# Kernel tuning notes

Hardware: AMD Instinct MI355X
Metric: run time of the kernel (lower is better)

## Reference

```python
import jax, jax.numpy as jnp
import numpy as np

B, T, M, D, H, DK, DV = 2, 1024, 1024, 1024, 16, 64, 64
R = 2 * T + M  # number of relative positions required by rel_shift path


def setup_inputs() -> dict:
    key = jax.random.key(0)
    ks = jax.random.split(key, 11)
    s = 0.02
    return {
        "inputs": jax.random.normal(ks[0], (B, T, D), jnp.float32),
        "attention_mask": jnp.ones((B, T, M + T), jnp.float32),
        "positional_encodings": jax.random.normal(ks[1], (R, D), jnp.float32),
        "memory": jax.random.normal(ks[2], (B, M, D), jnp.float32),
        "Wq": jax.random.normal(ks[3], (D, H * DK), jnp.float32) * s,
        "Wk": jax.random.normal(ks[4], (D, H * DK), jnp.float32) * s,
        "Wv": jax.random.normal(ks[5], (D, H * DV), jnp.float32) * s,
        "Wr": jax.random.normal(ks[6], (D, H * DK), jnp.float32) * s,
        "r_w_bias": jax.random.normal(ks[7], (H, DK), jnp.float32) * s,
        "r_r_bias": jax.random.normal(ks[8], (H, DK), jnp.float32) * s,
        "W_out": jax.random.normal(ks[9], (H * DV, D), jnp.float32) * s,
    }


def _rel_shift(m, attention_length):
    # m: [T_q, T_q + L] -> [T_q, L], TXL relative shift via reshape/slice
    tq, total = m.shape
    x = m.reshape(total, tq)[1:].reshape(tq, total - 1)
    return x[:, :attention_length]


def reference(inputs, attention_mask, positional_encodings, memory,
              Wq, Wk, Wv, Wr, r_w_bias, r_r_bias, W_out):
    b, t, d = inputs.shape
    values = jnp.concatenate([memory, inputs], axis=1)  # [B, L, D]
    L = values.shape[1]
    q = (inputs @ Wq).reshape(b, t, H, DK)
    k = (values @ Wk).reshape(b, L, H, DK)
    v = (values @ Wv).reshape(b, L, H, DV)
    rk = (positional_encodings @ Wr).reshape(-1, H, DK)  # [R, H, DK]
    # content + relative logits (TXL)
    content = jnp.einsum('bthd,bThd->bhtT', q + r_w_bias, k)        # [B,H,T,L]
    rel = jnp.einsum('bthd,rhd->bhtr', q + r_r_bias, rk)            # [B,H,T,R]
    rel = jax.vmap(jax.vmap(lambda m: _rel_shift(m, L)))(rel)       # [B,H,T,L]
    logits = (content + rel) * (DK ** -0.5)
    masked = logits - (1.0 - attention_mask[:, None, :, :]) * 1e30
    w = jax.nn.softmax(masked, axis=-1)
    attn = jnp.einsum('bhtT,bThd->bthd', w, v)                      # [B,T,H,DV]
    return attn.reshape(b, t, H * DV) @ W_out
```

## Files before the change

### kernel.cpp

```cpp
#include <hip/hip_runtime.h>
#include <stdint.h>

#define Bz 2
#define Tq 1024
#define Mm 1024
#define Hh 16
#define Ll 2048
#define Rr 3072

typedef __attribute__((ext_vector_type(8))) short bf16x8;
typedef __attribute__((ext_vector_type(4))) float f32x4;

typedef __attribute__((address_space(3))) uint8_t lds_u8_t;
typedef __attribute__((address_space(1))) uint8_t glb_u8_t;

__device__ __forceinline__ void gl2lds16(const void* g, void* l) {
  __builtin_amdgcn_global_load_lds((const glb_u8_t*)g, (lds_u8_t*)l, 16, 0, 0);
}

__device__ __forceinline__ unsigned short f2bf(float f) {
  unsigned int u = __builtin_bit_cast(unsigned int, f);
  u = u + 0x7fffu + ((u >> 16) & 1u);
  return (unsigned short)(u >> 16);
}
__device__ __forceinline__ float b2f(unsigned short s) {
  unsigned int u = ((unsigned int)s) << 16;
  return __builtin_bit_cast(float, u);
}

__global__ __launch_bounds__(256) void k_prep(const float* __restrict__ x,
                                              const float* __restrict__ mem,
                                              const float* __restrict__ pos,
                                              const float* __restrict__ mask,
                                              unsigned short* __restrict__ vin,
                                              unsigned short* __restrict__ pb,
                                              unsigned short* __restrict__ mb) {
  int bid = blockIdx.x;
  if (bid < 4096) {
    int idx = bid * 256 + threadIdx.x;
    int e = idx << 2;
    int row = e >> 10, col = e & 1023;
    int b = row >> 11, l = row & 2047;
    const float* s = (l < Mm) ? (mem + (((size_t)b * Mm + l) << 10) + col)
                              : (x + (((size_t)b * Tq + (l - Mm)) << 10) + col);
    float4 v = *(const float4*)s;
    ushort4 o;
    o.x = f2bf(v.x); o.y = f2bf(v.y); o.z = f2bf(v.z); o.w = f2bf(v.w);
    *(ushort4*)(vin + e) = o;
  } else if (bid < 7168) {
    int idx = (bid - 4096) * 256 + threadIdx.x;
    int e = idx << 2;
    float4 v = *(const float4*)(pos + e);
    ushort4 t;
    t.x = f2bf(v.x); t.y = f2bf(v.y); t.z = f2bf(v.z); t.w = f2bf(v.w);
    *(ushort4*)(pb + e) = t;
  } else {
    int idx = (bid - 7168) * 256 + threadIdx.x;
    int e = idx << 2;
    const float BIGM = 1.442695e30f;
    float4 v = *(const float4*)(mask + e);
    ushort4 t;
    t.x = f2bf((1.0f - v.x) * BIGM); t.y = f2bf((1.0f - v.y) * BIGM);
    t.z = f2bf((1.0f - v.z) * BIGM); t.w = f2bf((1.0f - v.w) * BIGM);
    *(ushort4*)(mb + e) = t;
  }
}

__global__ __launch_bounds__(256) void k_wtall(
    const float* __restrict__ w0, const float* __restrict__ w1,
    const float* __restrict__ w2, const float* __restrict__ w3,
    const float* __restrict__ w4,
    unsigned short* __restrict__ t0, unsigned short* __restrict__ t1,
    unsigned short* __restrict__ t2, unsigned short* __restrict__ t3,
    unsigned short* __restrict__ t4) {
  const float* W;
  unsigned short* WT;
  switch (blockIdx.z) {
    case 0: W = w0; WT = t0; break;
    case 1: W = w1; WT = t1; break;
    case 2: W = w2; WT = t2; break;
    case 3: W = w3; WT = t3; break;
    default: W = w4; WT = t4; break;
  }
  __shared__ float tile[64][65];
  int k0 = blockIdx.x * 64, n0 = blockIdx.y * 64;
  int tid = threadIdx.x;
  int rr = tid >> 4, c4 = (tid & 15) * 4;
#pragma unroll
  for (int it = 0; it < 4; ++it) {
    int r = rr + it * 16;
    float4 v = *(const float4*)(W + (size_t)(k0 + r) * 1024 + n0 + c4);
    tile[r][c4] = v.x; tile[r][c4 + 1] = v.y;
    tile[r][c4 + 2] = v.z; tile[r][c4 + 3] = v.w;
  }
  __syncthreads();
#pragma unroll
  for (int it = 0; it < 4; ++it) {
    int n = rr + it * 16;
    ushort4 o;
    o.x = f2bf(tile[c4 + 0][n]); o.y = f2bf(tile[c4 + 1][n]);
    o.z = f2bf(tile[c4 + 2][n]); o.w = f2bf(tile[c4 + 3][n]);
    *(ushort4*)(WT + (size_t)(n0 + n) * 1024 + k0 + c4) = o;
  }
}

template <int RMAP>
__device__ __forceinline__ void gemm_core(const unsigned short* __restrict__ A,
                                          const unsigned short* __restrict__ Bt,
                                          int m0, int n0, unsigned short* As,
                                          unsigned short* Bs, f32x4 acc[4][4]) {
  const int tid = threadIdx.x;
  const int w = tid >> 6, lane = tid & 63;
  const int quad = lane >> 4, li = lane & 15;
  const int wr = w >> 1, wc = w & 1;
  f32x4 z = {0.f, 0.f, 0.f, 0.f};
#pragma unroll
  for (int mi = 0; mi < 4; ++mi)
#pragma unroll
    for (int ni = 0; ni < 4; ++ni) acc[mi][ni] = z;

  const int rs = lane >> 2;
  const int cs = lane & 3;

  for (int k0 = 0; k0 < 1024; k0 += 32) {
    __syncthreads();
#pragma unroll
    for (int s = 0; s < 2; ++s) {
      int i = w * 2 + s;
      int r = i * 16 + rs;
      int c = cs ^ ((r >> 1) & 3);
      int ar = m0 + r;
      if (RMAP) ar = ar + 1024 + (ar & 1024);
      gl2lds16(A + (size_t)ar * 1024 + k0 + c * 8, (char*)As + i * 1024);
      int br = n0 + r;
      gl2lds16(Bt + (size_t)br * 1024 + k0 + c * 8, (char*)Bs + i * 1024);
    }
    __syncthreads();
    bf16x8 af[4], bfr[4];
#pragma unroll
    for (int mi = 0; mi < 4; ++mi) {
      int r = wr * 64 + mi * 16 + li;
      int ch = quad ^ ((r >> 1) & 3);
      af[mi] = *(const bf16x8*)((const char*)As + r * 64 + ch * 16);
    }
#pragma unroll
    for (int ni = 0; ni < 4; ++ni) {
      int r = wc * 64 + ni * 16 + li;
      int ch = quad ^ ((r >> 1) & 3);
      bfr[ni] = *(const bf16x8*)((const char*)Bs + r * 64 + ch * 16);
    }
#pragma unroll
    for (int mi = 0; mi < 4; ++mi)
#pragma unroll
      for (int ni = 0; ni < 4; ++ni)
        acc[mi][ni] = __builtin_amdgcn_mfma_f32_16x16x32_bf16(
            af[mi], bfr[ni], acc[mi][ni], 0, 0, 0);
  }
}

__global__ __launch_bounds__(256) void k_proj(
    const unsigned short* __restrict__ Vin, const unsigned short* __restrict__ Pb,
    const unsigned short* __restrict__ WqT, const unsigned short* __restrict__ WkT,
    const unsigned short* __restrict__ WvT, const unsigned short* __restrict__ WrT,
    const float* __restrict__ rwb, const float* __restrict__ rrb,
    unsigned short* __restrict__ qwb, unsigned short* __restrict__ qrb,
    unsigned short* __restrict__ kb, unsigned short* __restrict__ vtb,
    unsigned short* __restrict__ rkb) {
  __shared__ unsigned short As[128 * 32];
  __shared__ unsigned short Bs[128 * 32];
  const int t = blockIdx.x;
  const int tid = threadIdx.x, w = tid >> 6, lane = tid & 63;
  const int quad = lane >> 4, li = lane & 15, wr = w >> 1, wc = w & 1;
  f32x4 acc[4][4];

  if (t < 256) {
    int m0 = (t >> 3) * 128, n0 = (t & 7) * 128;
    gemm_core<0>(Vin, WkT, m0, n0, As, Bs, acc);
#pragma unroll
    for (int mi = 0; mi < 4; ++mi)
#pragma unroll
      for (int ni = 0; ni < 4; ++ni)
#pragma unroll
        for (int reg = 0; reg < 4; ++reg) {
          int rrow = m0 + wr * 64 + mi * 16 + quad * 4 + reg;
          int cc = n0 + wc * 64 + ni * 16 + li;
          kb[(size_t)rrow * 1024 + cc] = f2bf(acc[mi][ni][reg]);
        }
  } else if (t < 512) {
    int tt = t - 256;
    int m0 = (tt >> 3) * 128, n0 = (tt & 7) * 128;
    gemm_core<0>(Vin, WvT, m0, n0, As, Bs, acc);
#pragma unroll
    for (int mi = 0; mi < 4; ++mi)
#pragma unroll
      for (int ni = 0; ni < 4; ++ni) {
        int r0 = m0 + wr * 64 + mi * 16 + quad * 4;
        int b = r0 >> 11, l0 = r0 & 2047;
        int cc = n0 + wc * 64 + ni * 16 + li;
        ushort4 o;
        o.x = f2bf(acc[mi][ni][0]); o.y = f2bf(acc[mi][ni][1]);
        o.z = f2bf(acc[mi][ni][2]); o.w = f2bf(acc[mi][ni][3]);
        *(ushort4*)(vtb + ((size_t)(b * 1024 + cc)) * Ll + l0) = o;
      }
  } else if (t < 640) {
    int tt = t - 512;
    int m0 = (tt >> 3) * 128, n0 = (tt & 7) * 128;
    gemm_core<1>(Vin, WqT, m0, n0, As, Bs, acc);
#pragma unroll
    for (int mi = 0; mi < 4; ++mi)
#pragma unroll
      for (int ni = 0; ni < 4; ++ni) {
        int cc = n0 + wc * 64 + ni * 16 + li;
        float bw_ = rwb[cc], br_ = rrb[cc];
#pragma unroll
        for (int reg = 0; reg < 4; ++reg) {
          int rrow = m0 + wr * 64 + mi * 16 + quad * 4 + reg;
          size_t off = (size_t)rrow * 1024 + cc;
          qwb[off] = f2bf(acc[mi][ni][reg] + bw_);
          qrb[off] = f2bf(acc[mi][ni][reg] + br_);
        }
      }
  } else {
    int tt = t - 640;
    int m0 = (tt >> 3) * 128, n0 = (tt & 7) * 128;
    gemm_core<0>(Pb, WrT, m0, n0, As, Bs, acc);
#pragma unroll
    for (int mi = 0; mi < 4; ++mi)
#pragma unroll
      for (int ni = 0; ni < 4; ++ni)
#pragma unroll
        for (int reg = 0; reg < 4; ++reg) {
          int rrow = m0 + wr * 64 + mi * 16 + quad * 4 + reg;
          int cc = n0 + wc * 64 + ni * 16 + li;
          rkb[(size_t)rrow * 1024 + cc] = f2bf(acc[mi][ni][reg]);
        }
  }
}

__global__ __launch_bounds__(256) void k_gemm_out64(
    const unsigned short* __restrict__ attnb, const unsigned short* __restrict__ WoT,
    float* __restrict__ out) {
  __shared__ unsigned short As[64 * 32];
  __shared__ unsigned short Bs[128 * 32];
  int m0 = blockIdx.x * 64, n0 = blockIdx.y * 128;
  const int tid = threadIdx.x, w = tid >> 6, lane = tid & 63;
  const int quad = lane >> 4, li = lane & 15, wr = w >> 1, wc = w & 1;
  f32x4 z = {0.f, 0.f, 0.f, 0.f};
  f32x4 acc[2][4];
#pragma unroll
  for (int mi = 0; mi < 2; ++mi)
#pragma unroll
    for (int ni = 0; ni < 4; ++ni) acc[mi][ni] = z;
  const int rs = lane >> 2, cs = lane & 3;
  for (int k0 = 0; k0 < 1024; k0 += 32) {
    __syncthreads();
    {
      int r = w * 16 + rs;
      int c = cs ^ ((r >> 1) & 3);
      gl2lds16(attnb + (size_t)(m0 + r) * 1024 + k0 + c * 8, (char*)As + w * 1024);
    }
#pragma unroll
    for (int s = 0; s < 2; ++s) {
      int i = w * 2 + s;
      int r = i * 16 + rs;
      int c = cs ^ ((r >> 1) & 3);
      gl2lds16(WoT + (size_t)(n0 + r) * 1024 + k0 + c * 8, (char*)Bs + i * 1024);
    }
    __syncthreads();
    bf16x8 af[2], bfr[4];
#pragma unroll
    for (int mi = 0; mi < 2; ++mi) {
      int r = wr * 32 + mi * 16 + li;
      int ch = quad ^ ((r >> 1) & 3);
      af[mi] = *(const bf16x8*)((const char*)As + r * 64 + ch * 16);
    }
#pragma unroll
    for (int ni = 0; ni < 4; ++ni) {
      int r = wc * 64 + ni * 16 + li;
      int ch = quad ^ ((r >> 1) & 3);
      bfr[ni] = *(const bf16x8*)((const char*)Bs + r * 64 + ch * 16);
    }
#pragma unroll
    for (int mi = 0; mi < 2; ++mi)
#pragma unroll
      for (int ni = 0; ni < 4; ++ni)
        acc[mi][ni] = __builtin_amdgcn_mfma_f32_16x16x32_bf16(
            af[mi], bfr[ni], acc[mi][ni], 0, 0, 0);
  }
#pragma unroll
  for (int mi = 0; mi < 2; ++mi)
#pragma unroll
    for (int ni = 0; ni < 4; ++ni)
#pragma unroll
      for (int reg = 0; reg < 4; ++reg) {
        int rrow = m0 + wr * 32 + mi * 16 + quad * 4 + reg;
        int cc = n0 + wc * 64 + ni * 16 + li;
        out[(size_t)rrow * 1024 + cc] = acc[mi][ni][reg];
      }
}

__global__ __launch_bounds__(256, 3) void k_attn(
    const unsigned short* __restrict__ qw, const unsigned short* __restrict__ qr,
    const unsigned short* __restrict__ kb, const unsigned short* __restrict__ vt,
    const unsigned short* __restrict__ rkb, const unsigned short* __restrict__ mb,
    float* __restrict__ po, float* __restrict__ pl) {
  __shared__ unsigned short Ks[64 * 64];
  __shared__ unsigned short Vs[64 * 64];
  __shared__ unsigned short Rs[128 * 64];
  __shared__ unsigned short BndP[4][16 * 72];

  const int tid = threadIdx.x;
  const int w = tid >> 6, lane = tid & 63;
  const int quad = lane >> 4, li = lane & 15;
  const int qt = blockIdx.x, h = blockIdx.y;
  const int b = blockIdx.z >> 1, split = blockIdx.z & 1;
  const int t0blk = qt * 64;
  const int t0w = t0blk + w * 16;
  const int rboff = 48 - 16 * w;
  const int rbase0 = Tq - t0blk - 63 + (split << 10);

  bf16x8 aqw[2], aqr[2];
  {
    const unsigned short* p1 = qw + ((size_t)((b * Tq + t0w + li) * Hh + h)) * 64;
    aqw[0] = *(const bf16x8*)(p1 + quad * 8);
    aqw[1] = *(const bf16x8*)(p1 + 32 + quad * 8);
    const unsigned short* p2 = qr + ((size_t)((b * Tq + t0w + li) * Hh + h)) * 64;
    aqr[0] = *(const bf16x8*)(p2 + quad * 8);
    aqr[1] = *(const bf16x8*)(p2 + 32 + quad * 8);
  }

  f32x4 z = {0.f, 0.f, 0.f, 0.f};
  f32x4 o[4];
  o[0] = z; o[1] = z; o[2] = z; o[3] = z;
  f32x4 ol = z;

  const int srow = lane >> 3;
  const int scs = lane & 7;
  const float SC = 0.125f * 1.4426950408889634f;
  const short oneb = 0x3F80;
  const bf16x8 onesf = {oneb, oneb, oneb, oneb, oneb, oneb, oneb, oneb};

  unsigned short* pw = &BndP[w][0];

  for (int jt = 0; jt < 16; ++jt) {
    const int j0 = (split << 10) + jt * 64;
    __syncthreads();
#pragma unroll
    for (int s = 0; s < 2; ++s) {
      int i = w * 2 + s;
      int r = i * 8 + srow;
      int c = scs ^ (r & 7);
      gl2lds16(kb + ((size_t)((b * Ll + j0 + r) * Hh + h)) * 64 + c * 8,
               (char*)Ks + i * 1024);
      gl2lds16(vt + ((size_t)((b * Hh + h) * 64 + r)) * Ll + j0 + c * 8,
               (char*)Vs + i * 1024);
    }
    if (jt == 0) {
#pragma unroll
      for (int s = 0; s < 4; ++s) {
        int i = w * 4 + s;
        int r = i * 8 + srow;
        int gr = rbase0 + r;
        if (gr > Rr - 1) gr = Rr - 1;
        int c = scs ^ (r & 7);
        gl2lds16(rkb + ((size_t)gr * Hh + h) * 64 + c * 8, (char*)Rs + i * 1024);
      }
    } else {
      int ph0 = (64 * (jt + 1)) & 127;
#pragma unroll
      for (int s = 0; s < 2; ++s) {
        int i2 = w * 2 + s;
        int rr = i2 * 8 + srow;
        int gr = rbase0 + 64 * jt + 64 + rr;
        if (gr > Rr - 1) gr = Rr - 1;
        int c = scs ^ (rr & 7);
        gl2lds16(rkb + ((size_t)gr * Hh + h) * 64 + c * 8,
                 (char*)Rs + ph0 * 128 + i2 * 1024);
      }
    }
    __syncthreads();

    f32x4 sc[4];
    sc[0] = z; sc[1] = z; sc[2] = z; sc[3] = z;
#pragma unroll
    for (int ks = 0; ks < 2; ++ks)
#pragma unroll
      for (int nt = 0; nt < 4; ++nt) {
        int j = nt * 16 + li;
        int ch = (ks * 4 + quad) ^ (j & 7);
        bf16x8 kf = *(const bf16x8*)((const char*)Ks + j * 128 + ch * 16);
        sc[nt] = __builtin_amdgcn_mfma_f32_16x16x32_bf16(aqw[ks], kf, sc[nt], 0, 0, 0);
      }
    f32x4 bd[5];
    bd[0] = z; bd[1] = z; bd[2] = z; bd[3] = z; bd[4] = z;
#pragma unroll
    for (int ks = 0; ks < 2; ++ks)
#pragma unroll
      for (int nt = 0; nt < 5; ++nt) {
        int pr = (rboff + nt * 16 + li + 64 * jt) & 127;
        int ch = (ks * 4 + quad) ^ (pr & 7);
        bf16x8 rf = *(const bf16x8*)((const char*)Rs + pr * 128 + ch * 16);
        bd[nt] = __builtin_amdgcn_mfma_f32_16x16x32_bf16(aqr[ks], rf, bd[nt], 0, 0, 0);
      }
#pragma unroll
    for (int nt = 0; nt < 5; ++nt)
#pragma unroll
      for (int reg = 0; reg < 4; ++reg) {
        int row = quad * 4 + reg;
        int jj = nt * 16 + li + row - 15;
        if ((unsigned)jj < 64u) pw[row * 72 + jj] = f2bf(bd[nt][reg]);
      }
    __builtin_amdgcn_s_waitcnt(0xc07f);

    float pbuf[4][4];
    const unsigned short* mrow0 = mb + ((size_t)(b * Tq + t0w)) * Ll + j0;
#pragma unroll
    for (int nt = 0; nt < 4; ++nt)
#pragma unroll
      for (int reg = 0; reg < 4; ++reg) {
        int row = quad * 4 + reg;
        float rel = b2f(pw[row * 72 + nt * 16 + li]);
        float mv = b2f(mrow0[(size_t)row * Ll + nt * 16 + li]);
        float s = (sc[nt][reg] + rel) * SC - mv;
        pbuf[nt][reg] = exp2f(s);
      }
    asm volatile("" ::: "memory");
#pragma unroll
    for (int nt = 0; nt < 4; ++nt)
#pragma unroll
      for (int reg = 0; reg < 4; ++reg)
        pw[(quad * 4 + reg) * 72 + nt * 16 + li] = f2bf(pbuf[nt][reg]);
    __builtin_amdgcn_s_waitcnt(0xc07f);
#pragma unroll
    for (int ks = 0; ks < 2; ++ks) {
      bf16x8 ap = *(const bf16x8*)(pw + li * 72 + ks * 32 + quad * 8);
      ol = __builtin_amdgcn_mfma_f32_16x16x32_bf16(ap, onesf, ol, 0, 0, 0);
#pragma unroll
      for (int nt = 0; nt < 4; ++nt) {
        int dv = nt * 16 + li;
        int ch = (ks * 4 + quad) ^ (dv & 7);
        bf16x8 vf = *(const bf16x8*)((const char*)Vs + dv * 128 + ch * 16);
        o[nt] = __builtin_amdgcn_mfma_f32_16x16x32_bf16(ap, vf, o[nt], 0, 0, 0);
      }
    }
  }
  const int bs = (b * 2 + split) * 16 + h;
#pragma unroll
  for (int nt = 0; nt < 4; ++nt)
#pragma unroll
    for (int reg = 0; reg < 4; ++reg) {
      int trow = t0w + quad * 4 + reg;
      po[((size_t)bs * 1024 + trow) * 64 + nt * 16 + li] = o[nt][reg];
    }
  if (li == 0) {
#pragma unroll
    for (int reg = 0; reg < 4; ++reg) {
      int trow = t0w + quad * 4 + reg;
      pl[(size_t)bs * 1024 + trow] = ol[reg];
    }
  }
}

__global__ __launch_bounds__(256) void k_combine(
    const float* __restrict__ po, const float* __restrict__ pl,
    unsigned short* __restrict__ attnb) {
  int id = blockIdx.x * 256 + threadIdx.x;
  int dv4 = (id & 15) << 2;
  int t = (id >> 4) & 1023;
  int h = (id >> 14) & 15;
  int b = id >> 18;
  size_t r0 = ((size_t)((b * 2 + 0) * 16 + h)) * 1024 + t;
  size_t r1 = ((size_t)((b * 2 + 1) * 16 + h)) * 1024 + t;
  float inv = 1.0f / (pl[r0] + pl[r1]);
  float4 o0 = *(const float4*)(po + r0 * 64 + dv4);
  float4 o1 = *(const float4*)(po + r1 * 64 + dv4);
  ushort4 res;
  res.x = f2bf((o0.x + o1.x) * inv);
  res.y = f2bf((o0.y + o1.y) * inv);
  res.z = f2bf((o0.z + o1.z) * inv);
  res.w = f2bf((o0.w + o1.w) * inv);
  *(ushort4*)(attnb + ((size_t)(b * 1024 + t)) * 1024 + h * 64 + dv4) = res;
}

extern "C" void kernel_launch(void* const* d_in, const int* in_sizes, int n_in,
                              void* d_out, int out_size, void* d_ws, size_t ws_size,
                              hipStream_t stream) {
  const float* x = (const float*)d_in[0];
  const float* mask = (const float*)d_in[1];
  const float* pos = (const float*)d_in[2];
  const float* mem = (const float*)d_in[3];
  const float* Wq = (const float*)d_in[4];
  const float* Wk = (const float*)d_in[5];
  const float* Wv = (const float*)d_in[6];
  const float* Wr = (const float*)d_in[7];
  const float* rwb = (const float*)d_in[8];
  const float* rrb = (const float*)d_in[9];
  const float* Wo = (const float*)d_in[10];
  float* out = (float*)d_out;

  uint8_t* ws = (uint8_t*)d_ws;
  const size_t MB = 1024 * 1024;
  unsigned short* Vinb = (unsigned short*)(ws + 0);
  unsigned short* WqT = (unsigned short*)(ws + 8 * MB);
  unsigned short* WkT = (unsigned short*)(ws + 10 * MB);
  unsigned short* WvT = (unsigned short*)(ws + 12 * MB);
  unsigned short* WrT = (unsigned short*)(ws + 14 * MB);
  unsigned short* WoT = (unsigned short*)(ws + 16 * MB);
  unsigned short* Pb = (unsigned short*)(ws + 18 * MB);
  unsigned short* qwb = (unsigned short*)(ws + 24 * MB);
  unsigned short* qrb = (unsigned short*)(ws + 28 * MB);
  unsigned short* kb = (unsigned short*)(ws + 32 * MB);
  unsigned short* vtb = (unsigned short*)(ws + 40 * MB);
  unsigned short* rkb = (unsigned short*)(ws + 48 * MB);
  unsigned short* mbb = (unsigned short*)(ws + 54 * MB);
  float* po = (float*)(ws + 0);
  float* pl = (float*)(ws + 18 * MB);
  unsigned short* attnb = (unsigned short*)(ws + 19 * MB);

  hipLaunchKernelGGL(k_prep, dim3(11264), dim3(256), 0, stream,
                     x, mem, pos, mask, Vinb, Pb, mbb);
  hipLaunchKernelGGL(k_wtall, dim3(16, 16, 5), dim3(256), 0, stream,
                     Wq, Wk, Wv, Wr, Wo, WqT, WkT, WvT, WrT, WoT);
  hipLaunchKernelGGL(k_proj, dim3(832), dim3(256), 0, stream,
                     Vinb, Pb, WqT, WkT, WvT, WrT, rwb, rrb, qwb, qrb, kb, vtb, rkb);
  hipLaunchKernelGGL(k_attn, dim3(16, 16, 4), dim3(256), 0, stream,
                     qwb, qrb, kb, vtb, rkb, mbb, po, pl);
  hipLaunchKernelGGL(k_combine, dim3(2048), dim3(256), 0, stream, po, pl, attnb);
  hipLaunchKernelGGL(k_gemm_out64, dim3(32, 8), dim3(256), 0, stream,
                     attnb, WoT, out);
}
```

Baseline: 268.9 us.

## Fuse content and relative logits before LDS shift, compute softmax in A-operand layout

Content scores are rotated across lanes with shuffles so they line up with the shifted relative-position tile. The sum is then written to LDS once, as fp16, instead of writing only the relative part and reading it back. The exp2 and mask step now runs while the MFMA A-operand is loaded from LDS, using vectorised mask loads per row. This drops one LDS write/read round trip and a wait per tile, at the cost of extra shuffles and fp16 range limits on the pre-scaled logits.

```diff
diff --git a/kernel.cpp b/kernel.cpp
--- a/kernel.cpp
+++ b/kernel.cpp
@@ -1,4 +1,5 @@
 #include <hip/hip_runtime.h>
+#include <hip/hip_fp16.h>
 #include <stdint.h>
 
 #define Bz 2
@@ -307,7 +308,7 @@
   __shared__ unsigned short Ks[64 * 64];
   __shared__ unsigned short Vs[64 * 64];
   __shared__ unsigned short Rs[128 * 64];
-  __shared__ unsigned short BndP[4][16 * 72];
+  __shared__ unsigned short Sb[4][16 * 72];
 
   const int tid = threadIdx.x;
   const int w = tid >> 6, lane = tid & 63;
@@ -340,7 +341,14 @@
   const short oneb = 0x3F80;
   const bf16x8 onesf = {oneb, oneb, oneb, oneb, oneb, oneb, oneb, oneb};
 
-  unsigned short* pw = &BndP[w][0];
+  unsigned short* pw = &Sb[w][0];
+  const unsigned short* mrowA = mb + ((size_t)(b * Tq + t0w + li)) * Ll;
+  int srcl[4];
+#pragma unroll
+  for (int reg = 0; reg < 4; ++reg) {
+    int row = quad * 4 + reg;
+    srcl[reg] = (lane & 48) + ((li + row + 1) & 15);
+  }
 
   for (int jt = 0; jt < 16; ++jt) {
     const int j0 = (split << 10) + jt * 64;
@@ -402,38 +410,42 @@
         bf16x8 rf = *(const bf16x8*)((const char*)Rs + pr * 128 + ch * 16);
         bd[nt] = __builtin_amdgcn_mfma_f32_16x16x32_bf16(aqr[ks], rf, bd[nt], 0, 0, 0);
       }
+    float rot[4][4];
+#pragma unroll
+    for (int nt = 0; nt < 4; ++nt)
+#pragma unroll
+      for (int reg = 0; reg < 4; ++reg)
+        rot[nt][reg] = __shfl(sc[nt][reg], srcl[reg], 64);
 #pragma unroll
     for (int nt = 0; nt < 5; ++nt)
 #pragma unroll
       for (int reg = 0; reg < 4; ++reg) {
         int row = quad * 4 + reg;
         int jj = nt * 16 + li + row - 15;
-        if ((unsigned)jj < 64u) pw[row * 72 + jj] = f2bf(bd[nt][reg]);
+        int ntlo = (nt == 0) ? 3 : (nt - 1);
+        int nthi = (nt > 3) ? 0 : nt;
+        float val = ((li + row) >= 15) ? rot[nthi][reg] : rot[ntlo][reg];
+        float s = val + bd[nt][reg];
+        if ((unsigned)jj < 64u)
+          pw[row * 72 + jj] = __builtin_bit_cast(unsigned short, __float2half(s));
       }
     __builtin_amdgcn_s_waitcnt(0xc07f);
 
-    float pbuf[4][4];
-    const unsigned short* mrow0 = mb + ((size_t)(b * Tq + t0w)) * Ll + j0;
-#pragma unroll
-    for (int nt = 0; nt < 4; ++nt)
-#pragma unroll
-      for (int reg = 0; reg < 4; ++reg) {
-        int row = quad * 4 + reg;
-        float rel = b2f(pw[row * 72 + nt * 16 + li]);
-        float mv = b2f(mrow0[(size_t)row * Ll + nt * 16 + li]);
-        float s = (sc[nt][reg] + rel) * SC - mv;
-        pbuf[nt][reg] = exp2f(s);
-      }
-    asm volatile("" ::: "memory");
-#pragma unroll
-    for (int nt = 0; nt < 4; ++nt)
-#pragma unroll
-      for (int reg = 0; reg < 4; ++reg)
-        pw[(quad * 4 + reg) * 72 + nt * 16 + li] = f2bf(pbuf[nt][reg]);
-    __builtin_amdgcn_s_waitcnt(0xc07f);
 #pragma unroll
     for (int ks = 0; ks < 2; ++ks) {
-      bf16x8 ap = *(const bf16x8*)(pw + li * 72 + ks * 32 + quad * 8);
+      const int cofs = ks * 32 + quad * 8;
+      ushort4 s0 = *(const ushort4*)(pw + li * 72 + cofs);
+      ushort4 s1 = *(const ushort4*)(pw + li * 72 + cofs + 4);
+      bf16x8 mv = *(const bf16x8*)(mrowA + j0 + cofs);
+      unsigned short su[8] = {s0.x, s0.y, s0.z, s0.w, s1.x, s1.y, s1.z, s1.w};
+      bf16x8 ap;
+#pragma unroll
+      for (int i2 = 0; i2 < 8; ++i2) {
+        float sf = __half2float(__builtin_bit_cast(__half, su[i2]));
+        float mvf = b2f((unsigned short)mv[i2]);
+        float p = exp2f(sf * SC - mvf);
+        ap[i2] = (short)f2bf(p);
+      }
       ol = __builtin_amdgcn_mfma_f32_16x16x32_bf16(ap, onesf, ol, 0, 0, 0);
 #pragma unroll
       for (int nt = 0; nt < 4; ++nt) {
```

Measured after the change: 268.8 us. Within noise of the previous version (-0.0%).
